# Performance work log

Measured on AMD Instinct MI355X. Metric: run time of the kernel, lower is better.

## Reference

```python
import jax, jax.numpy as jnp
import numpy as np

L, B, D, H = 2048, 2, 1024, 16


def setup_inputs() -> dict:
    key = jax.random.key(0)
    ks = jax.random.split(key, 4)
    x = jax.random.normal(ks[0], (L, B, D), dtype=jnp.float32)
    W_in = jax.random.normal(ks[1], (3 * D, D), dtype=jnp.float32) * (1.0 / np.sqrt(D))
    b_in = jnp.zeros((3 * D,), dtype=jnp.float32)
    W_out = jax.random.normal(ks[2], (D, D), dtype=jnp.float32) * (1.0 / np.sqrt(D))
    b_out = jnp.zeros((D,), dtype=jnp.float32)
    mask = jnp.zeros((1, L, L), dtype=jnp.float32)
    return {"q": x, "k": x, "v": x, "mask": mask,
            "W_in": W_in, "b_in": b_in, "W_out": W_out, "b_out": b_out,
            "num_heads": H}


def reference(q, k, v, mask, W_in, b_in, W_out, b_out, num_heads):
    l, b, d = q.shape
    hd = d // num_heads
    # fused QKV projection (q == k == v in this module)
    qkv = q @ W_in.T + b_in                      # (l, b, 3d)
    qh, kh, vh = jnp.split(qkv, 3, axis=-1)      # each (l, b, d)

    def to_heads(t):
        # (l, b, d) -> (b*h, l, hd)
        return t.reshape(l, b * num_heads, hd).transpose(1, 0, 2)

    qh, kh, vh = to_heads(qh), to_heads(kh), to_heads(vh)
    qh = qh / jnp.sqrt(jnp.asarray(hd, dtype=qh.dtype))
    scores = jnp.einsum('nld,nmd->nlm', qh, kh) + mask   # (b*h, l, l)
    attn = jax.nn.softmax(scores, axis=-1)
    z = jnp.einsum('nlm,nmd->nld', attn, vh)             # (b*h, l, hd)
    z = z.transpose(1, 0, 2).reshape(l * b, d)
    z = z @ W_out.T + b_out
    return z.reshape(l, b, d)
```

## Files before the change

kernel.cpp:

```cpp
#include <hip/hip_runtime.h>


typedef short  s8v  __attribute__((ext_vector_type(8)));
typedef short  s4vv __attribute__((ext_vector_type(4)));
typedef float  f4v  __attribute__((ext_vector_type(4)));
typedef float  f4l  __attribute__((ext_vector_type(4)));
typedef float  f16v __attribute__((ext_vector_type(16)));
typedef int    i4v  __attribute__((ext_vector_type(4)));
typedef int    i2v  __attribute__((ext_vector_type(2)));

__device__ __forceinline__ short f2bf(float f) {
  union { float f; unsigned u; } x; x.f = f;
  unsigned r = (x.u + 0x7fffu + ((x.u >> 16) & 1u)) >> 16;
  return (short)r;
}

__device__ __forceinline__ int cvtpk(float lo, float hi) {
  int r;
  asm("v_cvt_pk_bf16_f32 %0, %1, %2" : "=v"(r) : "v"(lo), "v"(hi));
  return r;
}

#define GLDS16(gp, lp) __builtin_amdgcn_global_load_lds( \
    (const __attribute__((address_space(1))) void*)(gp),  \
    (__attribute__((address_space(3))) void*)(lp), 16, 0, 0)

#define LOG2E 1.4426950408889634f

__global__ __launch_bounds__(256) void prep(const float* __restrict__ x,
                                            const float* __restrict__ wi,
                                            const float* __restrict__ wo,
                                            const float* __restrict__ mask,
                                            short* __restrict__ xb,
                                            short* __restrict__ wib,
                                            short* __restrict__ wob,
                                            unsigned* __restrict__ flags) {
  const int b = blockIdx.x;
  if (b < 8192) {
    int i = b * 256 + threadIdx.x;
    const float* src; short* dst; int off;
    if (i < 1048576)               { src = x;  dst = xb;  off = i; }
    else if (i < 1048576 + 786432) { src = wi; dst = wib; off = i - 1048576; }
    else                           { src = wo; dst = wob; off = i - 1835008; }
    f4l v = ((const f4l*)src)[off];
    s4vv o;
    o[0] = f2bf(v[0]); o[1] = f2bf(v[1]); o[2] = f2bf(v[2]); o[3] = f2bf(v[3]);
    ((s4vv*)dst)[off] = o;
  } else {
    const int l = b - 8192;
    const int qt = l >> 7;
    const int t = threadIdx.x;
    const float* row = mask + ((size_t)l << 11) + (t << 3);
    f4l a = *(const f4l*)row;
    f4l bb = *(const f4l*)(row + 4);
    bool nz = (a[0] != 0.f) | (a[1] != 0.f) | (a[2] != 0.f) | (a[3] != 0.f) |
              (bb[0] != 0.f) | (bb[1] != 0.f) | (bb[2] != 0.f) | (bb[3] != 0.f);
    unsigned long long bal = __ballot(nz);
    const int w = t >> 6, lane = t & 63;
    if (lane == 0 && bal) {
      unsigned bits = 0;
#pragma unroll
      for (int g = 0; g < 8; ++g)
        if ((bal >> (g << 3)) & 0xFFull) bits |= 1u << ((w << 3) + g);
      atomicOr(&flags[qt], bits);
    }
  }
}

__global__ __launch_bounds__(256) void gemm_qkv(const short* __restrict__ A,
                                                const short* __restrict__ B,
                                                const float* __restrict__ bin,
                                                short* __restrict__ Qh,
                                                short* __restrict__ Kh,
                                                short* __restrict__ VT) {
  __shared__ __align__(16) short As[128 * 64];
  __shared__ __align__(16) short Bs[128 * 64];
  const int tid = threadIdx.x;
  const int w = tid >> 6, lane = tid & 63;
  const int g = lane >> 4, c15 = lane & 15;
  const int wr = w >> 1, wc = w & 1;
  const int orig = blockIdx.x;
  const int xcd = orig & 7, j6 = orig >> 3;
  const int bx = ((xcd & 1) * 12) + (j6 % 12);
  const int by = ((xcd >> 1) * 8) + (j6 / 12);
  const int rowbase = by << 7;
  const int colbase = bx << 7;
  const int rl = lane >> 3, sp = lane & 7;
  const int swz = (sp ^ rl) << 3;

  f4v acc[4][4] = {};

  for (int kt = 0; kt < 16; ++kt) {
#pragma unroll
    for (int c2 = 0; c2 < 4; ++c2) {
      const int chunk = (w << 2) + c2;
      const int row = (chunk << 3) + rl;
      GLDS16(A + ((size_t)(rowbase + row) << 10) + (kt << 6) + swz, &As[chunk << 9]);
      GLDS16(B + ((size_t)(colbase + row) << 10) + (kt << 6) + swz, &Bs[chunk << 9]);
    }
    __syncthreads();
#pragma unroll
    for (int kk = 0; kk < 2; ++kk) {
      s8v af[4], bf[4];
#pragma unroll
      for (int m = 0; m < 4; ++m) {
        const int row = (wr << 6) + (m << 4) + c15;
        af[m] = *(const s8v*)((const char*)As + row * 128 + ((((kk << 2) | g) ^ (row & 7)) << 4));
        const int col = (wc << 6) + (m << 4) + c15;
        bf[m] = *(const s8v*)((const char*)Bs + col * 128 + ((((kk << 2) | g) ^ (col & 7)) << 4));
      }
#pragma unroll
      for (int m = 0; m < 4; ++m)
#pragma unroll
        for (int nn = 0; nn < 4; ++nn)
          acc[m][nn] = __builtin_amdgcn_mfma_f32_16x16x32_bf16(af[m], bf[nn], acc[m][nn], 0, 0, 0);
    }
    __syncthreads();
  }

  const int r0 = rowbase + (wr << 6) + (g << 2);
  const int c0 = colbase + (wc << 6) + c15;
  const int which = colbase >> 10;
#pragma unroll
  for (int nn = 0; nn < 4; ++nn) {
    const int col = c0 + (nn << 4);
    const int dd = col & 1023;
    const int hh = dd >> 6, ee = dd & 63;
    const float bias = bin[col];
    if (which == 2) {
      unsigned* v0p = (unsigned*)(VT + ((((size_t)hh << 6) + ee) << 11));
      unsigned* v1p = (unsigned*)(VT + (((((size_t)hh + 16) << 6) + ee) << 11));
#pragma unroll
      for (int m = 0; m < 4; ++m) {
        const int li0 = (r0 >> 1) + (m << 3);
        v0p[li0 >> 1] = (unsigned)cvtpk(acc[m][nn][0] + bias, acc[m][nn][2] + bias);
        v1p[li0 >> 1] = (unsigned)cvtpk(acc[m][nn][1] + bias, acc[m][nn][3] + bias);
      }
    } else {
      const float mul = (which == 0) ? 0.125f * LOG2E : 1.0f;
      short* dst = (which == 0) ? Qh : Kh;
#pragma unroll
      for (int m = 0; m < 4; ++m) {
#pragma unroll
        for (int j = 0; j < 4; ++j) {
          const int row = r0 + (m << 4) + j;
          const int li = row >> 1, bb = row & 1;
          const int nh = (bb << 4) + hh;
          dst[(((size_t)nh * 2048 + li) << 6) + ee] = f2bf((acc[m][nn][j] + bias) * mul);
        }
      }
    }
  }
}

__global__ __launch_bounds__(256) void gemm_out(const short* __restrict__ A,
                                                const short* __restrict__ B,
                                                const float* __restrict__ bout,
                                                float* __restrict__ out) {
  __shared__ __align__(16) short As[128 * 64];
  __shared__ __align__(16) short Bs[64 * 64];
  const int tid = threadIdx.x;
  const int w = tid >> 6, lane = tid & 63;
  const int g = lane >> 4, c15 = lane & 15;
  const int orig = blockIdx.x;
  const int xcd = orig & 7, j6 = orig >> 3;
  const int colblk = (xcd << 1) + (j6 & 1);
  const int rowblk = j6 >> 1;
  const int rowbase = rowblk << 7;
  const int colbase = colblk << 6;
  const int rl = lane >> 3, sp = lane & 7;
  const int swz = (sp ^ rl) << 3;

  f4v acc[2][4] = {};

  for (int kt = 0; kt < 16; ++kt) {
#pragma unroll
    for (int c2 = 0; c2 < 4; ++c2) {
      const int chunk = (w << 2) + c2;
      const int row = (chunk << 3) + rl;
      GLDS16(A + ((size_t)(rowbase + row) << 10) + (kt << 6) + swz, &As[chunk << 9]);
    }
#pragma unroll
    for (int c2 = 0; c2 < 2; ++c2) {
      const int chunk = (w << 1) + c2;
      const int row = (chunk << 3) + rl;
      GLDS16(B + ((size_t)(colbase + row) << 10) + (kt << 6) + swz, &Bs[chunk << 9]);
    }
    __syncthreads();
#pragma unroll
    for (int kk = 0; kk < 2; ++kk) {
      s8v af[2], bf[4];
#pragma unroll
      for (int m = 0; m < 2; ++m) {
        const int row = (w << 5) + (m << 4) + c15;
        af[m] = *(const s8v*)((const char*)As + row * 128 + ((((kk << 2) | g) ^ (row & 7)) << 4));
      }
#pragma unroll
      for (int nn = 0; nn < 4; ++nn) {
        const int col = (nn << 4) + c15;
        bf[nn] = *(const s8v*)((const char*)Bs + col * 128 + ((((kk << 2) | g) ^ (col & 7)) << 4));
      }
#pragma unroll
      for (int m = 0; m < 2; ++m)
#pragma unroll
        for (int nn = 0; nn < 4; ++nn)
          acc[m][nn] = __builtin_amdgcn_mfma_f32_16x16x32_bf16(af[m], bf[nn], acc[m][nn], 0, 0, 0);
    }
    __syncthreads();
  }

  const int r0 = rowbase + (w << 5) + (g << 2);
  const int c0 = colbase + c15;
#pragma unroll
  for (int nn = 0; nn < 4; ++nn) {
    const int col = c0 + (nn << 4);
    const float bias = bout[col];
#pragma unroll
    for (int m = 0; m < 2; ++m) {
#pragma unroll
      for (int j = 0; j < 4; ++j) {
        const int row = r0 + (m << 4) + j;
        out[((size_t)row << 10) + col] = acc[m][nn][j] + bias;
      }
    }
  }
}

__global__ __launch_bounds__(256, 2) void attn(const short* __restrict__ Qh,
                                               const short* __restrict__ Kh,
                                               const short* __restrict__ VTg,
                                               const float* __restrict__ mask,
                                               const unsigned* __restrict__ mflags,
                                               short* __restrict__ Z) {
  __shared__ __align__(16) short Ks[2][128 * 64];
  __shared__ __align__(16) short Vs[2][64 * 128];
  const int tid = threadIdx.x;
  const int w = tid >> 6, lane = tid & 63;
  const int q5 = lane & 31, hi = lane >> 5;
  const int orig = blockIdx.x;
  const int wg = ((orig & 7) << 6) + (orig >> 3);
  const int n = wg >> 4, qt = wg & 15;
  const int krow8 = lane >> 3;
  const int ssw = ((lane & 7) ^ krow8) << 3;
  const int vrow = lane >> 4, vslot = lane & 15;

  const int qg = (qt << 7) + (w << 5) + q5;

  const short* Qp = Qh + (((size_t)n * 2048 + qg) << 6);
  s8v bq[4];
#pragma unroll
  for (int ks = 0; ks < 4; ++ks)
    bq[ks] = *(const s8v*)(Qp + (ks << 4) + (hi << 3));

  const short* Kbase = Kh + ((size_t)n << 17);
  const short* Vbase = VTg + ((size_t)n << 17);
  const float* mrow = mask + ((size_t)qg << 11) + (hi << 2);
  const unsigned mbits = mflags[qt];
  const int kslot = q5 & 7;
  const int vsl15 = q5 & 15;

  f16v oA0, oA1, zz;
#pragma unroll
  for (int e = 0; e < 16; ++e) { oA0[e] = 0.0f; oA1[e] = 0.0f; zz[e] = 0.0f; }
  float ls0 = 0.0f, ls1 = 0.0f;
  f16v sS[4];

#define STAGEK(bi, t) do {                                                      \
    _Pragma("unroll")                                                           \
    for (int c = 0; c < 4; ++c) {                                               \
      const int chunk = (w << 2) + c;                                           \
      GLDS16(Kbase + ((size_t)(((t) << 7) + (chunk << 3) + krow8) << 6) + ssw,  \
             &Ks[bi][chunk << 9]);                                              \
    } } while (0)
#define STAGEV(bi, t) do {                                                      \
    _Pragma("unroll")                                                           \
    for (int c = 0; c < 4; ++c) {                                               \
      const int chunk = (w << 2) + c;                                           \
      const int r = (chunk << 2) + vrow;                                        \
      GLDS16(Vbase + ((size_t)r << 11) + ((t) << 7) + ((vslot ^ (r & 15)) << 3),\
             &Vs[bi][chunk << 9]);                                              \
    } } while (0)

#define QKM(bi) do {                                                            \
    const char* Kc = (const char*)&Ks[bi][0];                                   \
    __builtin_amdgcn_s_setprio(1);                                              \
    _Pragma("unroll")                                                           \
    for (int ks = 0; ks < 4; ++ks) {                                            \
      const int so = ((2 * ks + hi) ^ kslot) << 4;                              \
      s8v a0 = *(const s8v*)(Kc + q5 * 128 + so);                               \
      s8v a1 = *(const s8v*)(Kc + (q5 + 32) * 128 + so);                        \
      s8v a2 = *(const s8v*)(Kc + (q5 + 64) * 128 + so);                        \
      s8v a3 = *(const s8v*)(Kc + (q5 + 96) * 128 + so);                        \
      if (ks == 0) {                                                            \
        sS[0] = __builtin_amdgcn_mfma_f32_32x32x16_bf16(a0, bq[0], zz, 0, 0, 0);\
        sS[1] = __builtin_amdgcn_mfma_f32_32x32x16_bf16(a1, bq[0], zz, 0, 0, 0);\
        sS[2] = __builtin_amdgcn_mfma_f32_32x32x16_bf16(a2, bq[0], zz, 0, 0, 0);\
        sS[3] = __builtin_amdgcn_mfma_f32_32x32x16_bf16(a3, bq[0], zz, 0, 0, 0);\
      } else {                                                                  \
        sS[0] = __builtin_amdgcn_mfma_f32_32x32x16_bf16(a0, bq[ks], sS[0], 0,0,0);\
        sS[1] = __builtin_amdgcn_mfma_f32_32x32x16_bf16(a1, bq[ks], sS[1], 0,0,0);\
        sS[2] = __builtin_amdgcn_mfma_f32_32x32x16_bf16(a2, bq[ks], sS[2], 0,0,0);\
        sS[3] = __builtin_amdgcn_mfma_f32_32x32x16_bf16(a3, bq[ks], sS[3], 0,0,0);\
      } }                                                                       \
    __builtin_amdgcn_s_setprio(0); } while (0)

#define SMPV(t, bi) do {                                                        \
    if ((mbits >> ((t) << 1)) & 1u) {                                           \
      const float* mp = mrow + ((t) << 7);                                      \
      _Pragma("unroll")                                                         \
      for (int c = 0; c < 4; ++c) {                                             \
        f4l m0 = *(const f4l*)(mp + (c << 3));                                  \
        f4l m1 = *(const f4l*)(mp + 32 + (c << 3));                             \
        _Pragma("unroll")                                                       \
        for (int jj = 0; jj < 4; ++jj) {                                        \
          sS[0][(c << 2) + jj] += m0[jj] * LOG2E;                               \
          sS[1][(c << 2) + jj] += m1[jj] * LOG2E;                               \
        } } }                                                                   \
    if ((mbits >> (((t) << 1) + 1)) & 1u) {                                     \
      const float* mp = mrow + ((t) << 7) + 64;                                 \
      _Pragma("unroll")                                                         \
      for (int c = 0; c < 4; ++c) {                                             \
        f4l m0 = *(const f4l*)(mp + (c << 3));                                  \
        f4l m1 = *(const f4l*)(mp + 32 + (c << 3));                             \
        _Pragma("unroll")                                                       \
        for (int jj = 0; jj < 4; ++jj) {                                        \
          sS[2][(c << 2) + jj] += m0[jj] * LOG2E;                               \
          sS[3][(c << 2) + jj] += m1[jj] * LOG2E;                               \
        } } }                                                                   \
    _Pragma("unroll")                                                           \
    for (int r = 0; r < 16; ++r) {                                              \
      float a = __builtin_amdgcn_exp2f(sS[0][r]); sS[0][r] = a; ls0 += a;       \
      float b = __builtin_amdgcn_exp2f(sS[1][r]); sS[1][r] = b; ls1 += b;       \
      float c = __builtin_amdgcn_exp2f(sS[2][r]); sS[2][r] = c; ls0 += c;       \
      float d = __builtin_amdgcn_exp2f(sS[3][r]); sS[3][r] = d; ls1 += d;       \
    }                                                                           \
    const char* Vc = (const char*)&Vs[bi][0];                                   \
    __builtin_amdgcn_s_setprio(1);                                              \
    _Pragma("unroll")                                                           \
    for (int kb = 0; kb < 4; ++kb) {                                            \
      _Pragma("unroll")                                                         \
      for (int ks2 = 0; ks2 < 2; ++ks2) {                                       \
        const int ro = ks2 << 3;                                                \
        int P0 = cvtpk(sS[kb][ro + 0], sS[kb][ro + 1]);                         \
        int P1 = cvtpk(sS[kb][ro + 2], sS[kb][ro + 3]);                         \
        int P2 = cvtpk(sS[kb][ro + 4], sS[kb][ro + 5]);                         \
        int P3 = cvtpk(sS[kb][ro + 6], sS[kb][ro + 7]);                         \
        int x0 = __shfl_xor(P2, 32);                                            \
        int x1 = __shfl_xor(P3, 32);                                            \
        int x2 = __shfl_xor(P0, 32);                                            \
        int x3 = __shfl_xor(P1, 32);                                            \
        union { i4v i; s8v s; } pu;                                             \
        pu.i[0] = hi ? x0 : P0;                                                 \
        pu.i[1] = hi ? x1 : P1;                                                 \
        pu.i[2] = hi ? P2 : x2;                                                 \
        pu.i[3] = hi ? P3 : x3;                                                 \
        const int p = (kb << 1) + ks2;                                          \
        const int so = (((p << 1) + hi) ^ vsl15) << 4;                          \
        s8v av0 = *(const s8v*)(Vc + q5 * 256 + so);                            \
        s8v av1 = *(const s8v*)(Vc + (q5 + 32) * 256 + so);                     \
        oA0 = __builtin_amdgcn_mfma_f32_32x32x16_bf16(av0, pu.s, oA0, 0, 0, 0); \
        oA1 = __builtin_amdgcn_mfma_f32_32x32x16_bf16(av1, pu.s, oA1, 0, 0, 0); \
      } }                                                                       \
    __builtin_amdgcn_s_setprio(0); } while (0)

  STAGEK(0, 0); STAGEV(0, 0);
  __syncthreads();

  for (int t = 0; t < 15; ++t) {
    STAGEK((t + 1) & 1, t + 1);
    STAGEV((t + 1) & 1, t + 1);
    QKM(t & 1);
    SMPV(t, t & 1);
    __syncthreads();
  }
  QKM(1);
  SMPV(15, 1);

#undef STAGEK
#undef STAGEV
#undef QKM
#undef SMPV

  float lrun = ls0 + ls1;
  lrun += __shfl_xor(lrun, 32);
  const float invl = 1.0f / lrun;
  short* zp = Z + ((((size_t)qg << 1) + (n >> 4)) << 10) + ((n & 15) << 6);
#pragma unroll
  for (int c = 0; c < 4; ++c) {
    const int d0 = (c << 3) + (hi << 2);
    i2v w0, w1;
    w0[0] = cvtpk(oA0[(c << 2) + 0] * invl, oA0[(c << 2) + 1] * invl);
    w0[1] = cvtpk(oA0[(c << 2) + 2] * invl, oA0[(c << 2) + 3] * invl);
    *(i2v*)(zp + d0) = w0;
    w1[0] = cvtpk(oA1[(c << 2) + 0] * invl, oA1[(c << 2) + 1] * invl);
    w1[1] = cvtpk(oA1[(c << 2) + 2] * invl, oA1[(c << 2) + 3] * invl);
    *(i2v*)(zp + 32 + d0) = w1;
  }
}

extern "C" void kernel_launch(void* const* d_in, const int* in_sizes, int n_in,
                              void* d_out, int out_size, void* d_ws, size_t ws_size,
                              hipStream_t stream) {
  const float* xq   = (const float*)d_in[0];
  const float* mask = (const float*)d_in[3];
  const float* Win  = (const float*)d_in[4];
  const float* bin  = (const float*)d_in[5];
  const float* Wout = (const float*)d_in[6];
  const float* bout = (const float*)d_in[7];
  float* out = (float*)d_out;

  char* ws = (char*)d_ws;
  short* xb  = (short*)(ws);
  short* wib = (short*)(ws + (8ull  << 20));
  short* wob = (short*)(ws + (14ull << 20));
  short* Qh  = (short*)(ws + (16ull << 20));
  short* Kh  = (short*)(ws + (24ull << 20));
  short* VTg = (short*)(ws + (32ull << 20));
  short* Zb  = (short*)(ws + (40ull << 20));
  unsigned* mflags = (unsigned*)(ws + (48ull << 20));

  hipMemsetAsync(mflags, 0, 16 * sizeof(unsigned), stream);
  prep<<<8192 + 2048, 256, 0, stream>>>(xq, Win, Wout, mask, xb, wib, wob, mflags);
  gemm_qkv<<<768, 256, 0, stream>>>(xb, wib, bin, Qh, Kh, VTg);
  attn<<<512, 256, 0, stream>>>(Qh, Kh, VTg, mask, mflags, Zb);
  gemm_out<<<512, 256, 0, stream>>>(Zb, wob, bout, out);
}
```

Before: 130.9 us.

## Enlarge QKV GEMM tiles to 256x256 with double-buffered LDS pipeline

The QKV projection GEMM moves from 128x128 tiles with 256 threads to 256x256 tiles with 512 threads (8 waves, 128x64 per wave). Global-to-LDS loads become double-buffered, prefetching the next K slice while the current one is computed, with explicit vmcnt waits and raw barriers. The goal is more data reuse per LDS load and hiding load latency behind the MFMA work. In exchange the grid shrinks to 192 blocks, fewer than the CU count, the XCD-aware block swizzle is dropped, and each block uses 128KB of LDS.

```diff
diff --git a/kernel.cpp b/kernel.cpp
--- a/kernel.cpp
+++ b/kernel.cpp
@@ -67,58 +67,76 @@
   }
 }
 
-__global__ __launch_bounds__(256) void gemm_qkv(const short* __restrict__ A,
-                                                const short* __restrict__ B,
-                                                const float* __restrict__ bin,
-                                                short* __restrict__ Qh,
-                                                short* __restrict__ Kh,
-                                                short* __restrict__ VT) {
-  __shared__ __align__(16) short As[128 * 64];
-  __shared__ __align__(16) short Bs[128 * 64];
+__global__ __launch_bounds__(512, 1) void gemm_qkv(const short* __restrict__ A,
+                                                   const short* __restrict__ B,
+                                                   const float* __restrict__ bin,
+                                                   short* __restrict__ Qh,
+                                                   short* __restrict__ Kh,
+                                                   short* __restrict__ VT) {
+  __shared__ __align__(16) short As[2][16384];
+  __shared__ __align__(16) short Bs[2][16384];
   const int tid = threadIdx.x;
   const int w = tid >> 6, lane = tid & 63;
   const int g = lane >> 4, c15 = lane & 15;
-  const int wr = w >> 1, wc = w & 1;
-  const int orig = blockIdx.x;
-  const int xcd = orig & 7, j6 = orig >> 3;
-  const int bx = ((xcd & 1) * 12) + (j6 % 12);
-  const int by = ((xcd >> 1) * 8) + (j6 / 12);
-  const int rowbase = by << 7;
-  const int colbase = bx << 7;
+  const int wr = w >> 2, wc = w & 3;
+  const int bx = blockIdx.x;
+  const int by = blockIdx.y;
+  const int rowbase = by << 8;
+  const int colbase = bx << 8;
   const int rl = lane >> 3, sp = lane & 7;
   const int swz = (sp ^ rl) << 3;
 
-  f4v acc[4][4] = {};
-
-  for (int kt = 0; kt < 16; ++kt) {
-#pragma unroll
-    for (int c2 = 0; c2 < 4; ++c2) {
-      const int chunk = (w << 2) + c2;
-      const int row = (chunk << 3) + rl;
-      GLDS16(A + ((size_t)(rowbase + row) << 10) + (kt << 6) + swz, &As[chunk << 9]);
-      GLDS16(B + ((size_t)(colbase + row) << 10) + (kt << 6) + swz, &Bs[chunk << 9]);
-    }
-    __syncthreads();
+  f4v acc[8][4] = {};
+
+#define VMW(N) asm volatile("s_waitcnt vmcnt(" #N ")" ::: "memory")
+#define BAR()  do { __builtin_amdgcn_s_barrier(); asm volatile("" ::: "memory"); } while (0)
+
+#define STAGE(bi, t) do {                                                        \
+    _Pragma("unroll")                                                            \
+    for (int c = 0; c < 4; ++c) {                                                \
+      const int chunk = (w << 2) + c;                                 \
+      const int row = (chunk << 3) + rl;                             \
+      GLDS16(A + ((size_t)(rowbase + row) << 10) + ((t) << 6) + swz,             \
+             &As[bi][chunk << 9]);                                               \
+      GLDS16(B + ((size_t)(colbase + row) << 10) + ((t) << 6) + swz,             \
+             &Bs[bi][chunk << 9]);                                               \
+    } } while (0)
+
+  STAGE(0, 0);
+
+#pragma unroll 1
+  for (int t = 0; t < 16; ++t) {
+    if (t < 15) { STAGE((t + 1) & 1, t + 1); VMW(8); }
+    else        { VMW(0); }
+    BAR();
+    const char* Ac = (const char*)&As[t & 1][0];
+    const char* Bc = (const char*)&Bs[t & 1][0];
 #pragma unroll
     for (int kk = 0; kk < 2; ++kk) {
-      s8v af[4], bf[4];
-#pragma unroll
-      for (int m = 0; m < 4; ++m) {
-        const int row = (wr << 6) + (m << 4) + c15;
-        af[m] = *(const s8v*)((const char*)As + row * 128 + ((((kk << 2) | g) ^ (row & 7)) << 4));
-        const int col = (wc << 6) + (m << 4) + c15;
-        bf[m] = *(const s8v*)((const char*)Bs + col * 128 + ((((kk << 2) | g) ^ (col & 7)) << 4));
-      }
-#pragma unroll
-      for (int m = 0; m < 4; ++m)
+      s8v af[8], bf[4];
+#pragma unroll
+      for (int m = 0; m < 8; ++m) {
+        const int row = (wr << 7) + (m << 4) + c15;
+        af[m] = *(const s8v*)(Ac + row * 128 + ((((kk << 2) | g) ^ (row & 7)) << 4));
+      }
+#pragma unroll
+      for (int nn = 0; nn < 4; ++nn) {
+        const int col = (wc << 6) + (nn << 4) + c15;
+        bf[nn] = *(const s8v*)(Bc + col * 128 + ((((kk << 2) | g) ^ (col & 7)) << 4));
+      }
+#pragma unroll
+      for (int m = 0; m < 8; ++m)
 #pragma unroll
         for (int nn = 0; nn < 4; ++nn)
           acc[m][nn] = __builtin_amdgcn_mfma_f32_16x16x32_bf16(af[m], bf[nn], acc[m][nn], 0, 0, 0);
     }
-    __syncthreads();
-  }
-
-  const int r0 = rowbase + (wr << 6) + (g << 2);
+    BAR();
+  }
+#undef STAGE
+#undef VMW
+#undef BAR
+
+  const int r0 = rowbase + (wr << 7) + (g << 2);
   const int c0 = colbase + (wc << 6) + c15;
   const int which = colbase >> 10;
 #pragma unroll
@@ -131,7 +149,7 @@
       unsigned* v0p = (unsigned*)(VT + ((((size_t)hh << 6) + ee) << 11));
       unsigned* v1p = (unsigned*)(VT + (((((size_t)hh + 16) << 6) + ee) << 11));
 #pragma unroll
-      for (int m = 0; m < 4; ++m) {
+      for (int m = 0; m < 8; ++m) {
         const int li0 = (r0 >> 1) + (m << 3);
         v0p[li0 >> 1] = (unsigned)cvtpk(acc[m][nn][0] + bias, acc[m][nn][2] + bias);
         v1p[li0 >> 1] = (unsigned)cvtpk(acc[m][nn][1] + bias, acc[m][nn][3] + bias);
@@ -140,7 +158,7 @@
       const float mul = (which == 0) ? 0.125f * LOG2E : 1.0f;
       short* dst = (which == 0) ? Qh : Kh;
 #pragma unroll
-      for (int m = 0; m < 4; ++m) {
+      for (int m = 0; m < 8; ++m) {
 #pragma unroll
         for (int j = 0; j < 4; ++j) {
           const int row = r0 + (m << 4) + j;
@@ -421,7 +439,7 @@
 
   hipMemsetAsync(mflags, 0, 16 * sizeof(unsigned), stream);
   prep<<<8192 + 2048, 256, 0, stream>>>(xq, Win, Wout, mask, xb, wib, wob, mflags);
-  gemm_qkv<<<768, 256, 0, stream>>>(xb, wib, bin, Qh, Kh, VTg);
+  gemm_qkv<<<dim3(12, 16), 512, 0, stream>>>(xb, wib, bin, Qh, Kh, VTg);
   attn<<<512, 256, 0, stream>>>(Qh, Kh, VTg, mask, mflags, Zb);
   gemm_out<<<512, 256, 0, stream>>>(Zb, wob, bout, out);
 }
```

Result: faster. 127.7 us (-2.4%).
